# Kernel tuning notes

Measured on AMD Instinct MI355X. Metric: run time of the kernel, lower is better.

## Reference

```python
import jax, jax.numpy as jnp
import numpy as np

EPS = 1e-12  # torch F.normalize eps


def rms_norm(x, g):
    # x: (b, c, l); normalize over channel dim, scale by g * sqrt(c)
    c = x.shape[1]
    n = jnp.sqrt(jnp.sum(x * x, axis=1, keepdims=True))
    return x / jnp.maximum(n, EPS) * g * jnp.sqrt(jnp.asarray(c, x.dtype))


def setup_inputs() -> dict:
    key = jax.random.key(0)
    ks = jax.random.split(key, 4)
    b, c, l = 4, 256, 2048
    heads, dim_head = 8, 64
    hidden = heads * dim_head
    x = jax.random.normal(ks[0], (b, c, l), dtype=jnp.float32)
    g1 = jnp.ones((1, c, 1), dtype=jnp.float32)
    w_qkv = jax.random.normal(ks[1], (hidden * 3, c), dtype=jnp.float32) * (c ** -0.5)
    w_out = jax.random.normal(ks[2], (c, hidden), dtype=jnp.float32) * (hidden ** -0.5)
    b_out = jnp.zeros((c,), dtype=jnp.float32)
    g2 = jnp.ones((1, c, 1), dtype=jnp.float32)
    return {"x": x, "g1": g1, "w_qkv": w_qkv, "w_out": w_out, "b_out": b_out, "g2": g2}


def reference(x, g1, w_qkv, w_out, b_out, g2):
    heads, dim_head = 8, 64
    scale = dim_head ** -0.5
    b, c, l = x.shape

    xn = rms_norm(x, g1)
    qkv = jnp.einsum('oc,bcl->bol', w_qkv, xn)  # (b, 3*hidden, l)
    q, k, v = jnp.split(qkv, 3, axis=1)
    # (b, h*d, l) -> (b, h, d, l)
    q = q.reshape(b, heads, dim_head, l) * scale
    k = k.reshape(b, heads, dim_head, l)
    v = v.reshape(b, heads, dim_head, l)

    sim = jnp.einsum('bhci,bhcj->bhij', q, k)          # (b, h, l, l)
    attn = jax.nn.softmax(sim, axis=-1)                # stable softmax (max-subtract)
    y = jnp.einsum('bhij,bhdj->bhid', attn, v)         # (b, h, l, d)

    # rearrange 'b h l d -> b (h d) l'
    y = jnp.transpose(y, (0, 1, 3, 2)).reshape(b, heads * dim_head, l)
    out = jnp.einsum('oc,bcl->bol', w_out, y) + b_out[None, :, None]
    return rms_norm(out, g2)
```

## Files before the change

### kernel.cpp

```cpp
#include <hip/hip_runtime.h>
#include <cstdint>
#include <cstddef>

using s16x4  = __attribute__((ext_vector_type(4))) short;
using short8 = __attribute__((ext_vector_type(8))) short;
using f32x4  = __attribute__((ext_vector_type(4))) float;
using f32x16 = __attribute__((ext_vector_type(16))) float;
using u32x4  = __attribute__((ext_vector_type(4))) unsigned int;

#define DEV static __device__ __forceinline__

constexpr int Bn = 4, Cn = 256, Ln = 2048, Hn = 8, Dn = 64, HIDn = 512;

DEV unsigned short f2bf(float f){
  union { float f; uint32_t u; } v; v.f = f;
  uint32_t u = v.u;
  return (unsigned short)((u + 0x7FFFu + ((u >> 16) & 1u)) >> 16);
}

DEV uint32_t cvtpk(float lo, float hi){
  uint32_t r;
  asm("v_cvt_pk_bf16_f32 %0, %1, %2" : "=v"(r) : "v"(lo), "v"(hi));
  return r;
}

DEV float fmax3(float a, float b, float c){ return fmaxf(fmaxf(a, b), c); }

DEV void gl16(const unsigned short* g, unsigned short* l){
  __builtin_amdgcn_global_load_lds((const __attribute__((address_space(1))) void*)g,
                                   (__attribute__((address_space(3))) void*)l, 16, 0, 0);
}

template<int NCHUNK>
DEV void stage_panel(const unsigned short* gbase, unsigned short* lbase, int tid, int wv){
  #pragma unroll
  for (int i = 0; i < NCHUNK; i += 256){
    int chunk = i + tid;
    int row = chunk >> 3, c = chunk & 7;
    gl16(gbase + (size_t)row * Cn + ((c ^ (row & 7)) * 8),
         lbase + (i + wv * 64) * 8);
  }
}

DEV short8 fragr(const char* base, int row, int ch){
  return *reinterpret_cast<const short8*>(base + row * 128 + ((ch ^ (row & 7)) << 4));
}

__global__ __launch_bounds__(256) void k_xt2(const float* __restrict__ x,
                                             const float* __restrict__ g1,
                                             unsigned short* __restrict__ xT,
                                             const float* __restrict__ wqkv,
                                             unsigned short* __restrict__ wqkv_b,
                                             const float* __restrict__ wout,
                                             unsigned short* __restrict__ wout_b){
  int bid = blockIdx.x;
  int tid = threadIdx.x;
  if (bid >= 128){
    if (bid < 512){
      int idx = (bid - 128) * 256 + tid;
      #pragma unroll
      for (int it = 0; it < 4; ++it){ wqkv_b[idx] = f2bf(wqkv[idx]); idx += 98304; }
    } else {
      int idx = (bid - 512) * 256 + tid;
      #pragma unroll
      for (int it = 0; it < 4; ++it){ wout_b[idx] = f2bf(wout[idx]); idx += 32768; }
    }
    return;
  }
  __shared__ float xs[4][64][65];
  __shared__ float ps[4][64];
  __shared__ float sl[64];
  int b  = bid >> 5;
  int l0 = (bid & 31) * 64;
  int i = tid >> 6, j = tid & 63;
  #pragma unroll
  for (int ct = 0; ct < 4; ++ct){
    const float* xp = x + ((size_t)(b * Cn + ct * 64) * Ln) + l0;
    #pragma unroll
    for (int it = 0; it < 16; ++it){
      int row = i + it * 4;
      xs[ct][row][j] = xp[(size_t)row * Ln + j];
    }
  }
  __syncthreads();
  {
    int lp = tid & 63, cq = tid >> 6;
    float a = 0.f;
    #pragma unroll 8
    for (int cc = 0; cc < 64; ++cc){ float v = xs[cq][cc][lp]; a += v * v; }
    ps[cq][lp] = a;
  }
  __syncthreads();
  if (tid < 64){
    float t = ps[0][tid] + ps[1][tid] + ps[2][tid] + ps[3][tid];
    sl[tid] = 16.0f / fmaxf(sqrtf(t), 1e-12f);
  }
  __syncthreads();
  int jj = tid >> 2, part = tid & 3;
  float sc = sl[jj];
  #pragma unroll
  for (int ct = 0; ct < 4; ++ct){
    unsigned short* op = xT + ((size_t)(b * Ln + l0 + jj)) * Cn + ct * 64 + part * 16;
    #pragma unroll
    for (int hb = 0; hb < 2; ++hb){
      short8 pack;
      #pragma unroll
      for (int m = 0; m < 8; ++m){
        int c = part * 16 + hb * 8 + m;
        pack[m] = (short)f2bf(xs[ct][c][jj] * sc * g1[ct * 64 + c]);
      }
      *reinterpret_cast<short8*>(op + hb * 8) = pack;
    }
  }
}

__global__ __launch_bounds__(256) void k_gemm_qkv(const unsigned short* __restrict__ xT,
                                                  const unsigned short* __restrict__ w,
                                                  unsigned short* __restrict__ qb,
                                                  unsigned short* __restrict__ kb,
                                                  unsigned short* __restrict__ vb){
  __shared__ alignas(16) char smem[49152];
  int b  = blockIdx.z;
  int l0 = blockIdx.x * 128;
  int tid = threadIdx.x;
  int wv = tid >> 6, lane = tid & 63;
  int grp = lane >> 4, lc = lane & 15;
  const unsigned short* xb = xT + (size_t)b * Ln * Cn;

  if (blockIdx.y < 16){
    int n0 = blockIdx.y * 64;
    int lwl = (wv >> 1) * 64, nwl = (wv & 1) * 32;
    unsigned short* As = (unsigned short*)smem;
    unsigned short* Bs = (unsigned short*)(smem + 32768);
    f32x4 acc[4][2] = {};
    stage_panel<1024>(xb + (size_t)l0 * Cn, As, tid, wv);
    stage_panel<512> (w  + (size_t)n0 * Cn, Bs, tid, wv);
    asm volatile("s_waitcnt vmcnt(0)" ::: "memory");
    __syncthreads();
    #pragma unroll
    for (int s = 0; s < 4; ++s){
      if (s < 3){
        stage_panel<1024>(xb + (size_t)l0 * Cn + (s + 1) * 64, As + ((s + 1) & 1) * 8192, tid, wv);
        stage_panel<512> (w  + (size_t)n0 * Cn + (s + 1) * 64, Bs + ((s + 1) & 1) * 4096, tid, wv);
      }
      const char* Ab = (const char*)(As + (s & 1) * 8192);
      const char* Bb = (const char*)(Bs + (s & 1) * 4096);
      #pragma unroll
      for (int kk = 0; kk < 2; ++kk){
        short8 afr[4], bfr[2];
        #pragma unroll
        for (int mt = 0; mt < 4; ++mt) afr[mt] = fragr(Ab, lwl + mt * 16 + lc, kk * 4 + grp);
        #pragma unroll
        for (int nt = 0; nt < 2; ++nt) bfr[nt] = fragr(Bb, nwl + nt * 16 + lc, kk * 4 + grp);
        #pragma unroll
        for (int mt = 0; mt < 4; ++mt)
          #pragma unroll
          for (int nt = 0; nt < 2; ++nt)
            acc[mt][nt] = __builtin_amdgcn_mfma_f32_16x16x32_bf16(afr[mt], bfr[nt], acc[mt][nt], 0, 0, 0);
      }
      asm volatile("s_waitcnt vmcnt(0)" ::: "memory");
      __syncthreads();
    }
    const float QSCALE = 0.125f * 1.4426950408889634f;
    #pragma unroll
    for (int mt = 0; mt < 4; ++mt)
      #pragma unroll
      for (int nt = 0; nt < 2; ++nt)
        #pragma unroll
        for (int r = 0; r < 4; ++r){
          int l = l0 + lwl + mt * 16 + grp * 4 + r;
          int o = n0 + nwl + nt * 16 + lc;
          float v = acc[mt][nt][r];
          if (o < HIDn){
            size_t idx = (((size_t)(b * Hn + (o >> 6)) * Ln + l) << 6) | (size_t)(o & 63);
            qb[idx] = f2bf(v * QSCALE);
          } else {
            int o2 = o - HIDn;
            size_t idx = (((size_t)(b * Hn + (o2 >> 6)) * Ln + l) << 6) | (size_t)(o2 & 63);
            kb[idx] = f2bf(v);
          }
        }
  } else {
    int m0 = (blockIdx.y - 16) * 64;
    int mwl = (wv >> 1) * 32, lwl = (wv & 1) * 64;
    const unsigned short* wvp = w + (size_t)1024 * Cn;
    unsigned short* Av = (unsigned short*)smem;
    unsigned short* Bv = (unsigned short*)(smem + 16384);
    f32x4 acc[2][4] = {};
    stage_panel<512> (wvp + (size_t)m0 * Cn, Av, tid, wv);
    stage_panel<1024>(xb  + (size_t)l0 * Cn, Bv, tid, wv);
    asm volatile("s_waitcnt vmcnt(0)" ::: "memory");
    __syncthreads();
    #pragma unroll
    for (int s = 0; s < 4; ++s){
      if (s < 3){
        stage_panel<512> (wvp + (size_t)m0 * Cn + (s + 1) * 64, Av + ((s + 1) & 1) * 4096, tid, wv);
        stage_panel<1024>(xb  + (size_t)l0 * Cn + (s + 1) * 64, Bv + ((s + 1) & 1) * 8192, tid, wv);
      }
      const char* Ab = (const char*)(Av + (s & 1) * 4096);
      const char* Bb = (const char*)(Bv + (s & 1) * 8192);
      #pragma unroll
      for (int kk = 0; kk < 2; ++kk){
        short8 afr[2], bfr[4];
        #pragma unroll
        for (int mt = 0; mt < 2; ++mt) afr[mt] = fragr(Ab, mwl + mt * 16 + lc, kk * 4 + grp);
        #pragma unroll
        for (int nt = 0; nt < 4; ++nt) bfr[nt] = fragr(Bb, lwl + nt * 16 + lc, kk * 4 + grp);
        #pragma unroll
        for (int mt = 0; mt < 2; ++mt)
          #pragma unroll
          for (int nt = 0; nt < 4; ++nt)
            acc[mt][nt] = __builtin_amdgcn_mfma_f32_16x16x32_bf16(afr[mt], bfr[nt], acc[mt][nt], 0, 0, 0);
      }
      asm volatile("s_waitcnt vmcnt(0)" ::: "memory");
      __syncthreads();
    }
    #pragma unroll
    for (int mt = 0; mt < 2; ++mt)
      #pragma unroll
      for (int nt = 0; nt < 4; ++nt)
        #pragma unroll
        for (int r = 0; r < 4; ++r){
          int o = m0 + mwl + mt * 16 + grp * 4 + r;
          int l = l0 + lwl + nt * 16 + lc;
          vb[((size_t)(b * HIDn + o)) * Ln + l] = f2bf(acc[mt][nt][r]);
        }
  }
}

__global__ __launch_bounds__(256) void k_attn(const unsigned short* __restrict__ qb,
                                              const unsigned short* __restrict__ kb,
                                              const unsigned short* __restrict__ vb,
                                              unsigned short* __restrict__ yb){
  int wid = (blockIdx.x & 7) * 64 + (blockIdx.x >> 3);
  int qt = wid & 15;
  int bh = wid >> 4;
  int b = bh >> 3, h = bh & 7;
  int tid = threadIdx.x;
  int wv = tid >> 6, lane = tid & 63;
  int ln = lane & 31, hi = lane >> 5;

  const unsigned short* qp = qb + (size_t)bh * Ln * Dn;
  const unsigned short* kp = kb + (size_t)bh * Ln * Dn;
  const unsigned short* vp = vb + ((size_t)(b * HIDn + h * Dn)) * Ln;
  unsigned short* yp = yb + (size_t)b * Ln * HIDn + h * Dn;

  __shared__ alignas(16) unsigned short KV[4][2][4096];

  int lrow = lane >> 3, lcol = lane & 7;
  int chunk = lcol ^ lrow;
  int srow = wv * 16 + lrow;
  const unsigned short* kg = kp + (size_t)srow * Dn + chunk * 8;
  const unsigned short* vg = vp + (size_t)srow * Ln + chunk * 8;
  int ldK = wv * 1024;

  int q = qt * 128 + wv * 32 + ln;
  int sw = (ln & 7) << 4;

  f32x16 accO[2] = {};
  f32x16 sA[2], sB[2];
  float m = -1e30f;
  float lsv[16] = {};
  const f32x16 ZV = {};

  auto DMA = [&](int tile, int buf){
    const unsigned short* kgn = kg + (size_t)tile * 64 * Dn;
    const unsigned short* vgn = vg + (size_t)tile * 64;
    unsigned short* Kd = &KV[buf][0][ldK];
    unsigned short* Vd = &KV[buf][1][ldK];
    gl16(kgn,          Kd);
    gl16(kgn + 8 * Dn, Kd + 512);
    gl16(vgn,          Vd);
    gl16(vgn + 8 * Ln, Vd + 512);
  };

  DMA(0, 0);
  DMA(1, 1);
  short8 qf[4];
  #pragma unroll
  for (int s = 0; s < 4; ++s)
    qf[s] = *reinterpret_cast<const short8*>(qp + (size_t)q * Dn + s * 16 + hi * 8);
  asm volatile("s_waitcnt vmcnt(4)" ::: "memory");
  __builtin_amdgcn_s_barrier();
  DMA(2, 2);

  {
    const char* Kc = (const char*)&KV[0][0][0];
    sA[0] = ZV; sA[1] = ZV;
    #pragma unroll
    for (int kb2 = 0; kb2 < 2; ++kb2){
      const char* Kr = Kc + (kb2 * 32 + ln) * 128;
      #pragma unroll
      for (int s = 0; s < 4; ++s){
        short8 kf = *reinterpret_cast<const short8*>(Kr + ((s * 32 + hi * 16) ^ sw));
        sA[kb2] = __builtin_amdgcn_mfma_f32_32x32x16_bf16(kf, qf[s], sA[kb2], 0, 0, 0);
      }
    }
  }

  auto ITER = [&](int t, f32x16 (&sC)[2], f32x16 (&sN)[2]){
    int tl = t + 3; if (tl > 31) tl = 31;
    DMA(tl, (t + 3) & 3);

    if (t + 1 < 32){
      const char* Kc = (const char*)&KV[(t + 1) & 3][0][0];
      sN[0] = ZV; sN[1] = ZV;
      __builtin_amdgcn_s_setprio(1);
      #pragma unroll
      for (int kb2 = 0; kb2 < 2; ++kb2){
        const char* Kr = Kc + (kb2 * 32 + ln) * 128;
        #pragma unroll
        for (int s = 0; s < 4; ++s){
          short8 kf = *reinterpret_cast<const short8*>(Kr + ((s * 32 + hi * 16) ^ sw));
          sN[kb2] = __builtin_amdgcn_mfma_f32_32x32x16_bf16(kf, qf[s], sN[kb2], 0, 0, 0);
        }
      }
      __builtin_amdgcn_s_setprio(0);
    }

    float mx[8];
    #pragma unroll
    for (int r = 0; r < 8; ++r)
      mx[r] = fmaxf(fmaxf(sC[0][r], sC[0][r + 8]), fmaxf(sC[1][r], sC[1][r + 8]));
    float pl = fmax3(fmax3(mx[0], mx[1], mx[2]),
                     fmax3(mx[3], mx[4], mx[5]),
                     fmaxf(mx[6], mx[7]));
    float pmax = fmaxf(pl, __shfl_xor(pl, 32, 64));

    if (!__all(pmax - m <= 8.0f)){
      float mn = fmaxf(m, pmax);
      float corr = exp2f(m - mn);
      #pragma unroll
      for (int r = 0; r < 16; ++r) lsv[r] *= corr;
      #pragma unroll
      for (int db = 0; db < 2; ++db)
        #pragma unroll
        for (int r = 0; r < 16; ++r) accO[db][r] *= corr;
      m = mn;
    }

    #pragma unroll
    for (int r = 0; r < 16; ++r){
      float p0, p1;
      asm("v_exp_f32 %0, %1" : "=v"(p0) : "v"(sC[0][r] - m));
      asm("v_exp_f32 %0, %1" : "=v"(p1) : "v"(sC[1][r] - m));
      sC[0][r] = p0; sC[1][r] = p1;
      lsv[r] += p0 + p1;
    }

    const char* Vc = (const char*)&KV[t & 3][1][0];
    __builtin_amdgcn_s_setprio(1);
    #pragma unroll
    for (int c = 0; c < 4; ++c){
      int base = (c & 1) * 8, kb2 = c >> 1;
      u32x4 W;
      W[0] = cvtpk(sC[kb2][base + 0], sC[kb2][base + 1]);
      W[1] = cvtpk(sC[kb2][base + 2], sC[kb2][base + 3]);
      W[2] = cvtpk(sC[kb2][base + 4], sC[kb2][base + 5]);
      W[3] = cvtpk(sC[kb2][base + 6], sC[kb2][base + 7]);
      short8 Bf = __builtin_bit_cast(short8, W);
      #pragma unroll
      for (int db = 0; db < 2; ++db){
        const char* Vr = Vc + (db * 32 + ln) * 128;
        s16x4 a0 = *reinterpret_cast<const s16x4*>(Vr + ((c * 32) ^ sw) + hi * 8);
        s16x4 a1 = *reinterpret_cast<const s16x4*>(Vr + ((c * 32 + 16) ^ sw) + hi * 8);
        short8 Af = {a0[0], a0[1], a0[2], a0[3], a1[0], a1[1], a1[2], a1[3]};
        accO[db] = __builtin_amdgcn_mfma_f32_32x32x16_bf16(Af, Bf, accO[db], 0, 0, 0);
      }
    }
    __builtin_amdgcn_s_setprio(0);

    asm volatile("s_waitcnt vmcnt(4)" ::: "memory");
    __builtin_amdgcn_s_barrier();
  };

  for (int t = 0; t < 32; t += 2){
    ITER(t,     sA, sB);
    ITER(t + 1, sB, sA);
  }

  #pragma unroll
  for (int st = 8; st >= 1; st >>= 1)
    #pragma unroll
    for (int r = 0; r < st; ++r) lsv[r] += lsv[r + st];
  float lsum = lsv[0] + __shfl_xor(lsv[0], 32, 64);
  float inv = 1.0f / lsum;
  #pragma unroll
  for (int db = 0; db < 2; ++db)
    #pragma unroll
    for (int rq = 0; rq < 4; ++rq){
      uint32_t w0 = cvtpk(accO[db][rq * 4 + 0] * inv, accO[db][rq * 4 + 1] * inv);
      uint32_t w1 = cvtpk(accO[db][rq * 4 + 2] * inv, accO[db][rq * 4 + 3] * inv);
      int dd = db * 32 + rq * 8 + hi * 4;
      uint32_t* dst = reinterpret_cast<uint32_t*>(yp + (size_t)q * HIDn + dd);
      dst[0] = w0; dst[1] = w1;
    }
}

__global__ __launch_bounds__(256) void k_out(const unsigned short* __restrict__ yb,
                                             const unsigned short* __restrict__ w,
                                             const float* __restrict__ bias,
                                             const float* __restrict__ g2,
                                             float* __restrict__ out){
  int b  = blockIdx.y;
  int l0 = blockIdx.x * 16;
  int wv = threadIdx.x >> 6, lane = threadIdx.x & 63;
  int grp = lane >> 4, lc = lane & 15;
  int mw = wv * 64;
  f32x4 acc[4] = {};
  const unsigned short* ybp = yb + (size_t)b * Ln * HIDn + (size_t)l0 * HIDn;
  for (int k0 = 0; k0 < HIDn; k0 += 32){
    int kc = k0 + grp * 8;
    short8 afr[4], bfr;
    #pragma unroll
    for (int mt = 0; mt < 4; ++mt)
      afr[mt] = *reinterpret_cast<const short8*>(w + (size_t)(mw + mt * 16 + lc) * HIDn + kc);
    bfr = *reinterpret_cast<const short8*>(ybp + (size_t)lc * HIDn + kc);
    #pragma unroll
    for (int mt = 0; mt < 4; ++mt)
      acc[mt] = __builtin_amdgcn_mfma_f32_16x16x32_bf16(afr[mt], bfr, acc[mt], 0, 0, 0);
  }
  __shared__ float cs[4][16];
  __shared__ float sc2[16];
  float part = 0.f;
  #pragma unroll
  for (int mt = 0; mt < 4; ++mt)
    #pragma unroll
    for (int r = 0; r < 4; ++r){
      int o = mw + mt * 16 + grp * 4 + r;
      float v = acc[mt][r] + bias[o];
      acc[mt][r] = v;
      part += v * v;
    }
  part += __shfl_xor(part, 16, 64);
  part += __shfl_xor(part, 32, 64);
  if (lane < 16) cs[wv][lc] = part;
  __syncthreads();
  if (threadIdx.x < 16){
    float t = cs[0][threadIdx.x] + cs[1][threadIdx.x] + cs[2][threadIdx.x] + cs[3][threadIdx.x];
    sc2[threadIdx.x] = 16.0f / fmaxf(sqrtf(t), 1e-12f);
  }
  __syncthreads();
  float s2 = sc2[lc];
  #pragma unroll
  for (int mt = 0; mt < 4; ++mt)
    #pragma unroll
    for (int r = 0; r < 4; ++r){
      int o = mw + mt * 16 + grp * 4 + r;
      int l = l0 + lc;
      out[((size_t)(b * Cn + o)) * Ln + l] = acc[mt][r] * s2 * g2[o];
    }
}

extern "C" void kernel_launch(void* const* d_in, const int* in_sizes, int n_in,
                              void* d_out, int out_size, void* d_ws, size_t ws_size,
                              hipStream_t stream){
  const float* x     = (const float*)d_in[0];
  const float* g1    = (const float*)d_in[1];
  const float* w_qkv = (const float*)d_in[2];
  const float* w_out = (const float*)d_in[3];
  const float* b_out = (const float*)d_in[4];
  const float* g2    = (const float*)d_in[5];

  char* wsb = (char*)d_ws;
  unsigned short* wqkv_b = (unsigned short*)(wsb + 0);
  unsigned short* wout_b = (unsigned short*)(wsb + 786432);
  unsigned short* xT     = (unsigned short*)(wsb + 1081344);
  unsigned short* qbuf   = (unsigned short*)(wsb + 5275648);
  unsigned short* kbuf   = (unsigned short*)(wsb + 13664256);
  unsigned short* vbuf   = (unsigned short*)(wsb + 22052864);
  unsigned short* ybuf   = (unsigned short*)(wsb + 30441472);

  k_xt2<<<640, 256, 0, stream>>>(x, g1, xT, w_qkv, wqkv_b, w_out, wout_b);
  k_gemm_qkv<<<dim3(16, 24, 4), 256, 0, stream>>>(xT, wqkv_b, qbuf, kbuf, vbuf);
  k_attn<<<512, 256, 0, stream>>>(qbuf, kbuf, vbuf, ybuf);
  k_out<<<dim3(128, 4), 256, 0, stream>>>(ybuf, wout_b, b_out, g2, (float*)d_out);
}
```

Baseline: 96.97 us.

## Software-pipeline attention PV behind QK, add occupancy hint, stage out-proj weights in LDS

The attention loop is reordered so each iteration computes QK for the next tile, then PV for the previous tile using packed probabilities kept in registers, then the softmax for the current tile. This lets MFMA work overlap the softmax. The K/V prefetch distance drops from 3 to 2, waits become full vmcnt(0), and launch bounds request 2 blocks per SM. The output projection now stages the weight matrix through double-buffered swizzled LDS instead of reading it straight from global per wave, which adds barriers and uses 64KB of LDS per block.

```diff
diff --git a/kernel.cpp b/kernel.cpp
--- a/kernel.cpp
+++ b/kernel.cpp
@@ -31,13 +31,13 @@
                                    (__attribute__((address_space(3))) void*)l, 16, 0, 0);
 }
 
-template<int NCHUNK>
+template<int NCHUNK, int RS>
 DEV void stage_panel(const unsigned short* gbase, unsigned short* lbase, int tid, int wv){
   #pragma unroll
   for (int i = 0; i < NCHUNK; i += 256){
     int chunk = i + tid;
     int row = chunk >> 3, c = chunk & 7;
-    gl16(gbase + (size_t)row * Cn + ((c ^ (row & 7)) * 8),
+    gl16(gbase + (size_t)row * RS + ((c ^ (row & 7)) * 8),
          lbase + (i + wv * 64) * 8);
   }
 }
@@ -133,15 +133,15 @@
     unsigned short* As = (unsigned short*)smem;
     unsigned short* Bs = (unsigned short*)(smem + 32768);
     f32x4 acc[4][2] = {};
-    stage_panel<1024>(xb + (size_t)l0 * Cn, As, tid, wv);
-    stage_panel<512> (w  + (size_t)n0 * Cn, Bs, tid, wv);
+    stage_panel<1024, Cn>(xb + (size_t)l0 * Cn, As, tid, wv);
+    stage_panel<512,  Cn>(w  + (size_t)n0 * Cn, Bs, tid, wv);
     asm volatile("s_waitcnt vmcnt(0)" ::: "memory");
     __syncthreads();
     #pragma unroll
     for (int s = 0; s < 4; ++s){
       if (s < 3){
-        stage_panel<1024>(xb + (size_t)l0 * Cn + (s + 1) * 64, As + ((s + 1) & 1) * 8192, tid, wv);
-        stage_panel<512> (w  + (size_t)n0 * Cn + (s + 1) * 64, Bs + ((s + 1) & 1) * 4096, tid, wv);
+        stage_panel<1024, Cn>(xb + (size_t)l0 * Cn + (s + 1) * 64, As + ((s + 1) & 1) * 8192, tid, wv);
+        stage_panel<512,  Cn>(w  + (size_t)n0 * Cn + (s + 1) * 64, Bs + ((s + 1) & 1) * 4096, tid, wv);
       }
       const char* Ab = (const char*)(As + (s & 1) * 8192);
       const char* Bb = (const char*)(Bs + (s & 1) * 4096);
@@ -187,15 +187,15 @@
     unsigned short* Av = (unsigned short*)smem;
     unsigned short* Bv = (unsigned short*)(smem + 16384);
     f32x4 acc[2][4] = {};
-    stage_panel<512> (wvp + (size_t)m0 * Cn, Av, tid, wv);
-    stage_panel<1024>(xb  + (size_t)l0 * Cn, Bv, tid, wv);
+    stage_panel<512,  Cn>(wvp + (size_t)m0 * Cn, Av, tid, wv);
+    stage_panel<1024, Cn>(xb  + (size_t)l0 * Cn, Bv, tid, wv);
     asm volatile("s_waitcnt vmcnt(0)" ::: "memory");
     __syncthreads();
     #pragma unroll
     for (int s = 0; s < 4; ++s){
       if (s < 3){
-        stage_panel<512> (wvp + (size_t)m0 * Cn + (s + 1) * 64, Av + ((s + 1) & 1) * 4096, tid, wv);
-        stage_panel<1024>(xb  + (size_t)l0 * Cn + (s + 1) * 64, Bv + ((s + 1) & 1) * 8192, tid, wv);
+        stage_panel<512,  Cn>(wvp + (size_t)m0 * Cn + (s + 1) * 64, Av + ((s + 1) & 1) * 4096, tid, wv);
+        stage_panel<1024, Cn>(xb  + (size_t)l0 * Cn + (s + 1) * 64, Bv + ((s + 1) & 1) * 8192, tid, wv);
       }
       const char* Ab = (const char*)(Av + (s & 1) * 4096);
       const char* Bb = (const char*)(Bv + (s & 1) * 8192);
@@ -228,10 +228,10 @@
   }
 }
 
-__global__ __launch_bounds__(256) void k_attn(const unsigned short* __restrict__ qb,
-                                              const unsigned short* __restrict__ kb,
-                                              const unsigned short* __restrict__ vb,
-                                              unsigned short* __restrict__ yb){
+__global__ __launch_bounds__(256, 2) void k_attn(const unsigned short* __restrict__ qb,
+                                                 const unsigned short* __restrict__ kb,
+                                                 const unsigned short* __restrict__ vb,
+                                                 unsigned short* __restrict__ yb){
   int wid = (blockIdx.x & 7) * 64 + (blockIdx.x >> 3);
   int qt = wid & 15;
   int bh = wid >> 4;
@@ -259,6 +259,7 @@
 
   f32x16 accO[2] = {};
   f32x16 sA[2], sB[2];
+  u32x4 Wsv[4];
   float m = -1e30f;
   float lsv[16] = {};
   const f32x16 ZV = {};
@@ -280,44 +281,44 @@
   #pragma unroll
   for (int s = 0; s < 4; ++s)
     qf[s] = *reinterpret_cast<const short8*>(qp + (size_t)q * Dn + s * 16 + hi * 8);
-  asm volatile("s_waitcnt vmcnt(4)" ::: "memory");
+  asm volatile("s_waitcnt vmcnt(0)" ::: "memory");
   __builtin_amdgcn_s_barrier();
-  DMA(2, 2);
-
-  {
-    const char* Kc = (const char*)&KV[0][0][0];
-    sA[0] = ZV; sA[1] = ZV;
+
+  auto QK = [&](int buf, f32x16 (&sN)[2]){
+    const char* Kc = (const char*)&KV[buf][0][0];
+    sN[0] = ZV; sN[1] = ZV;
+    __builtin_amdgcn_s_setprio(1);
     #pragma unroll
     for (int kb2 = 0; kb2 < 2; ++kb2){
       const char* Kr = Kc + (kb2 * 32 + ln) * 128;
       #pragma unroll
       for (int s = 0; s < 4; ++s){
         short8 kf = *reinterpret_cast<const short8*>(Kr + ((s * 32 + hi * 16) ^ sw));
-        sA[kb2] = __builtin_amdgcn_mfma_f32_32x32x16_bf16(kf, qf[s], sA[kb2], 0, 0, 0);
-      }
-    }
-  }
-
-  auto ITER = [&](int t, f32x16 (&sC)[2], f32x16 (&sN)[2]){
-    int tl = t + 3; if (tl > 31) tl = 31;
-    DMA(tl, (t + 3) & 3);
-
-    if (t + 1 < 32){
-      const char* Kc = (const char*)&KV[(t + 1) & 3][0][0];
-      sN[0] = ZV; sN[1] = ZV;
-      __builtin_amdgcn_s_setprio(1);
-      #pragma unroll
-      for (int kb2 = 0; kb2 < 2; ++kb2){
-        const char* Kr = Kc + (kb2 * 32 + ln) * 128;
-        #pragma unroll
-        for (int s = 0; s < 4; ++s){
-          short8 kf = *reinterpret_cast<const short8*>(Kr + ((s * 32 + hi * 16) ^ sw));
-          sN[kb2] = __builtin_amdgcn_mfma_f32_32x32x16_bf16(kf, qf[s], sN[kb2], 0, 0, 0);
-        }
-      }
-      __builtin_amdgcn_s_setprio(0);
-    }
-
+        sN[kb2] = __builtin_amdgcn_mfma_f32_32x32x16_bf16(kf, qf[s], sN[kb2], 0, 0, 0);
+      }
+    }
+    __builtin_amdgcn_s_setprio(0);
+  };
+
+  auto PV = [&](int tprev){
+    const char* Vc = (const char*)&KV[tprev & 3][1][0];
+    __builtin_amdgcn_s_setprio(1);
+    #pragma unroll
+    for (int c = 0; c < 4; ++c){
+      short8 Bf = __builtin_bit_cast(short8, Wsv[c]);
+      #pragma unroll
+      for (int db = 0; db < 2; ++db){
+        const char* Vr = Vc + (db * 32 + ln) * 128;
+        s16x4 a0 = *reinterpret_cast<const s16x4*>(Vr + ((c * 32) ^ sw) + hi * 8);
+        s16x4 a1 = *reinterpret_cast<const s16x4*>(Vr + ((c * 32 + 16) ^ sw) + hi * 8);
+        short8 Af = {a0[0], a0[1], a0[2], a0[3], a1[0], a1[1], a1[2], a1[3]};
+        accO[db] = __builtin_amdgcn_mfma_f32_32x32x16_bf16(Af, Bf, accO[db], 0, 0, 0);
+      }
+    }
+    __builtin_amdgcn_s_setprio(0);
+  };
+
+  auto SM = [&](f32x16 (&sC)[2]){
     float mx[8];
     #pragma unroll
     for (int r = 0; r < 8; ++r)
@@ -347,30 +348,25 @@
       sC[0][r] = p0; sC[1][r] = p1;
       lsv[r] += p0 + p1;
     }
-
-    const char* Vc = (const char*)&KV[t & 3][1][0];
-    __builtin_amdgcn_s_setprio(1);
     #pragma unroll
     for (int c = 0; c < 4; ++c){
       int base = (c & 1) * 8, kb2 = c >> 1;
-      u32x4 W;
-      W[0] = cvtpk(sC[kb2][base + 0], sC[kb2][base + 1]);
-      W[1] = cvtpk(sC[kb2][base + 2], sC[kb2][base + 3]);
-      W[2] = cvtpk(sC[kb2][base + 4], sC[kb2][base + 5]);
-      W[3] = cvtpk(sC[kb2][base + 6], sC[kb2][base + 7]);
-      short8 Bf = __builtin_bit_cast(short8, W);
-      #pragma unroll
-      for (int db = 0; db < 2; ++db){
-        const char* Vr = Vc + (db * 32 + ln) * 128;
-        s16x4 a0 = *reinterpret_cast<const s16x4*>(Vr + ((c * 32) ^ sw) + hi * 8);
-        s16x4 a1 = *reinterpret_cast<const s16x4*>(Vr + ((c * 32 + 16) ^ sw) + hi * 8);
-        short8 Af = {a0[0], a0[1], a0[2], a0[3], a1[0], a1[1], a1[2], a1[3]};
-        accO[db] = __builtin_amdgcn_mfma_f32_32x32x16_bf16(Af, Bf, accO[db], 0, 0, 0);
-      }
-    }
-    __builtin_amdgcn_s_setprio(0);
-
-    asm volatile("s_waitcnt vmcnt(4)" ::: "memory");
+      Wsv[c][0] = cvtpk(sC[kb2][base + 0], sC[kb2][base + 1]);
+      Wsv[c][1] = cvtpk(sC[kb2][base + 2], sC[kb2][base + 3]);
+      Wsv[c][2] = cvtpk(sC[kb2][base + 4], sC[kb2][base + 5]);
+      Wsv[c][3] = cvtpk(sC[kb2][base + 6], sC[kb2][base + 7]);
+    }
+  };
+
+  QK(0, sA);
+
+  auto ITER = [&](int t, f32x16 (&sC)[2], f32x16 (&sN)[2]){
+    int tl = t + 2 > 31 ? 31 : t + 2;
+    DMA(tl, (t + 2) & 3);
+    if (t + 1 < 32) QK((t + 1) & 3, sN);
+    if (t > 0)      PV(t - 1);
+    SM(sC);
+    asm volatile("s_waitcnt vmcnt(0)" ::: "memory");
     __builtin_amdgcn_s_barrier();
   };
 
@@ -378,6 +374,7 @@
     ITER(t,     sA, sB);
     ITER(t + 1, sB, sA);
   }
+  PV(31);
 
   #pragma unroll
   for (int st = 8; st >= 1; st >>= 1)
@@ -402,26 +399,40 @@
                                              const float* __restrict__ bias,
                                              const float* __restrict__ g2,
                                              float* __restrict__ out){
+  __shared__ alignas(16) unsigned short Ws[2][16384];
+  __shared__ float cs[4][16];
+  __shared__ float sc2[16];
   int b  = blockIdx.y;
   int l0 = blockIdx.x * 16;
-  int wv = threadIdx.x >> 6, lane = threadIdx.x & 63;
+  int tid = threadIdx.x;
+  int wv = tid >> 6, lane = tid & 63;
   int grp = lane >> 4, lc = lane & 15;
   int mw = wv * 64;
   f32x4 acc[4] = {};
   const unsigned short* ybp = yb + (size_t)b * Ln * HIDn + (size_t)l0 * HIDn;
-  for (int k0 = 0; k0 < HIDn; k0 += 32){
-    int kc = k0 + grp * 8;
-    short8 afr[4], bfr;
-    #pragma unroll
-    for (int mt = 0; mt < 4; ++mt)
-      afr[mt] = *reinterpret_cast<const short8*>(w + (size_t)(mw + mt * 16 + lc) * HIDn + kc);
-    bfr = *reinterpret_cast<const short8*>(ybp + (size_t)lc * HIDn + kc);
-    #pragma unroll
-    for (int mt = 0; mt < 4; ++mt)
-      acc[mt] = __builtin_amdgcn_mfma_f32_16x16x32_bf16(afr[mt], bfr, acc[mt], 0, 0, 0);
-  }
-  __shared__ float cs[4][16];
-  __shared__ float sc2[16];
+
+  stage_panel<2048, HIDn>(w, Ws[0], tid, wv);
+  asm volatile("s_waitcnt vmcnt(0)" ::: "memory");
+  __syncthreads();
+  #pragma unroll
+  for (int s = 0; s < 8; ++s){
+    if (s < 7) stage_panel<2048, HIDn>(w + (s + 1) * 64, Ws[(s + 1) & 1], tid, wv);
+    const char* Ab = (const char*)Ws[s & 1];
+    #pragma unroll
+    for (int kk = 0; kk < 2; ++kk){
+      int kc = s * 64 + kk * 32 + grp * 8;
+      short8 afr[4];
+      #pragma unroll
+      for (int mt = 0; mt < 4; ++mt) afr[mt] = fragr(Ab, mw + mt * 16 + lc, kk * 4 + grp);
+      short8 bfr = *reinterpret_cast<const short8*>(ybp + (size_t)lc * HIDn + kc);
+      #pragma unroll
+      for (int mt = 0; mt < 4; ++mt)
+        acc[mt] = __builtin_amdgcn_mfma_f32_16x16x32_bf16(afr[mt], bfr, acc[mt], 0, 0, 0);
+    }
+    asm volatile("s_waitcnt vmcnt(0)" ::: "memory");
+    __syncthreads();
+  }
+
   float part = 0.f;
   #pragma unroll
   for (int mt = 0; mt < 4; ++mt)
@@ -436,9 +447,9 @@
   part += __shfl_xor(part, 32, 64);
   if (lane < 16) cs[wv][lc] = part;
   __syncthreads();
-  if (threadIdx.x < 16){
-    float t = cs[0][threadIdx.x] + cs[1][threadIdx.x] + cs[2][threadIdx.x] + cs[3][threadIdx.x];
-    sc2[threadIdx.x] = 16.0f / fmaxf(sqrtf(t), 1e-12f);
+  if (tid < 16){
+    float t = cs[0][tid] + cs[1][tid] + cs[2][tid] + cs[3][tid];
+    sc2[tid] = 16.0f / fmaxf(sqrtf(t), 1e-12f);
   }
   __syncthreads();
   float s2 = sc2[lc];
```

Measured after the change: 86.22 us. 1.12x faster.
